# Performance work log

Hardware: AMD Instinct MI355X
Metric: run time of the kernel (lower is better)

## Reference

```python
import jax, jax.numpy as jnp
import numpy as np

WIDTH = 768
HEAD = 64

def setup_inputs() -> dict:
    key = jax.random.key(0)
    ks = jax.random.split(key, 8)
    x = jax.random.normal(ks[0], (8, 2048, WIDTH), dtype=jnp.float32)
    mask = jax.random.randint(ks[1], (2048, 2048), 0, 2, dtype=jnp.int32)
    s = 1.0 / np.sqrt(WIDTH)
    Wq = jax.random.normal(ks[2], (WIDTH, HEAD), dtype=jnp.float32) * s
    Wk = jax.random.normal(ks[3], (WIDTH, HEAD), dtype=jnp.float32) * s
    Wv = jax.random.normal(ks[4], (WIDTH, HEAD), dtype=jnp.float32) * s
    bq = jax.random.normal(ks[5], (HEAD,), dtype=jnp.float32) * 0.01
    bk = jax.random.normal(ks[6], (HEAD,), dtype=jnp.float32) * 0.01
    bv = jax.random.normal(ks[7], (HEAD,), dtype=jnp.float32) * 0.01
    return {"x": x, "Wq": Wq, "bq": bq, "Wk": Wk, "bk": bk, "Wv": Wv, "bv": bv, "mask": mask}

def reference(x, Wq, bq, Wk, bk, Wv, bv, mask) -> jnp.ndarray:
    # x: [B, N, width]; projections -> [B, N, head]
    Q = jnp.einsum('bnw,wh->bnh', x, Wq) + bq
    K = jnp.einsum('bnw,wh->bnh', x, Wk) + bk
    V = jnp.einsum('bnw,wh->bnh', x, Wv) + bv
    scale = 1.0 / jnp.sqrt(jnp.asarray(Q.shape[-1], dtype=Q.dtype))
    scores = jnp.einsum('bqh,bkh->bqk', Q, K) * scale  # [B, N, N]
    scores = jnp.where(mask == 0, -jnp.inf, scores)
    attn = jax.nn.softmax(scores, axis=-1)
    return jnp.einsum('bqk,bkh->bqh', attn, V)
```

## Files before the change

kernel.cpp:

```cpp
#include <hip/hip_runtime.h>

typedef short  s8v   __attribute__((ext_vector_type(8)));
typedef float  f32x4 __attribute__((ext_vector_type(4)));

#define SEQ 2048
#define WID 768

__device__ __forceinline__ unsigned fbits(float f) {
    union { float f; unsigned u; } v; v.f = f; return v.u;
}
__device__ __forceinline__ float bitsf(unsigned u) {
    union { unsigned u; float f; } v; v.u = u; return v.f;
}
__device__ __forceinline__ unsigned short f2b(float f) {
    unsigned u = fbits(f);
    return (unsigned short)((u + 0x7FFFu + ((u >> 16) & 1u)) >> 16);
}
__device__ __forceinline__ unsigned packRNE(float a, float b) {
    unsigned ta = fbits(a) + 0x7FFFu + ((fbits(a) >> 16) & 1u);
    unsigned tb = fbits(b) + 0x7FFFu + ((fbits(b) >> 16) & 1u);
    return __builtin_amdgcn_perm(tb, ta, 0x07060302u);
}
__device__ __forceinline__ unsigned packTRUNC(float a, float b) {
    return __builtin_amdgcn_perm(fbits(b), fbits(a), 0x07060302u);
}
__device__ __forceinline__ f32x4 zero4() { f32x4 z = {0.f, 0.f, 0.f, 0.f}; return z; }

__device__ __forceinline__ void async16(const unsigned short* g, unsigned short* l) {
    __builtin_amdgcn_global_load_lds(
        (const __attribute__((address_space(1))) unsigned int*)g,
        (__attribute__((address_space(3))) unsigned int*)l, 16, 0, 0);
}

__global__ __launch_bounds__(256) void convert_kernel(
    const int* __restrict__ mask,
    const float* __restrict__ Wq, const float* __restrict__ Wk, const float* __restrict__ Wv,
    unsigned short* __restrict__ WF, unsigned* __restrict__ PM)
{
    const int tid = threadIdx.x;
    const int blk = blockIdx.x;
    if (blk < 512) {
        const int gid  = blk * 4 + (tid >> 6);
        const int lane = tid & 63, quad = lane >> 4, c = lane & 15;
        const int qb = gid >> 5, kb = gid & 31;
        unsigned w = 0;
        #pragma unroll
        for (int mt = 0; mt < 2; ++mt) {
            const int q = qb * 32 + mt * 16 + c;
            #pragma unroll
            for (int i = 0; i < 4; ++i) {
                const int4 mm = *(const int4*)&mask[(size_t)q * SEQ + kb * 64 + quad * 16 + 4 * i];
                if (mm.x) w |= 1u << (mt * 16 + i * 4 + 0);
                if (mm.y) w |= 1u << (mt * 16 + i * 4 + 1);
                if (mm.z) w |= 1u << (mt * 16 + i * 4 + 2);
                if (mm.w) w |= 1u << (mt * 16 + i * 4 + 3);
            }
        }
        PM[(size_t)gid * 64 + lane] = w;
    } else {
        const int s2 = (blk - 512) * 256 + tid;
        const int chunk = s2 >> 6, l = s2 & 63;
        const int ntg = chunk / 24, r = chunk - ntg * 24;
        const int kc = r >> 1, h = r & 1;
        const int mat = ntg >> 2;
        const int col = (ntg & 3) * 16 + (l & 15);
        const int k0 = kc * 64 + h * 32 + (l >> 4) * 8;
        const float* Wm = (mat == 0) ? Wq : (mat == 1) ? Wk : Wv;
        float p[8];
        #pragma unroll
        for (int j = 0; j < 8; ++j) p[j] = Wm[(size_t)(k0 + j) * 64 + col];
        uint4 w;
        w.x = packRNE(p[0], p[1]); w.y = packRNE(p[2], p[3]);
        w.z = packRNE(p[4], p[5]); w.w = packRNE(p[6], p[7]);
        *(uint4*)&WF[(size_t)s2 * 8] = w;
    }
}

__global__ __launch_bounds__(512, 4) void qkv_proj_kernel(
    const float* __restrict__ x, const unsigned short* __restrict__ WF,
    const float* __restrict__ bq, const float* __restrict__ bk, const float* __restrict__ bv,
    unsigned short* __restrict__ QF, unsigned short* __restrict__ KF,
    unsigned short* __restrict__ VF)
{
    __shared__ unsigned short AB[2][14336];
    unsigned short (*St)[200] = (unsigned short(*)[200])AB;

    const int tid = threadIdx.x;
    const int wv = tid >> 6, lane = tid & 63, quad = lane >> 4, c = lane & 15;
    const int rg = wv >> 2, cg = wv & 3;
    const int blk = blockIdx.x;
    const int bsw = blk & 7, tsw = blk >> 3;
    const int kbt2 = bsw * 64 + tsw;
    const int kbt  = kbt2 >> 1, hb = kbt2 & 1;
    const int g0r  = kbt2 * 2;

    float bias[3];
    #pragma unroll
    for (int nt = 0; nt < 3; ++nt) {
        int col = cg * 48 + nt * 16 + c;
        const float* B = (col < 64) ? bq : (col < 128) ? bk : bv;
        bias[nt] = B[col & 63];
    }

    const int ach = tid >> 7;
    const int agl = ach >> 1, ah = ach & 1;
    const int al  = (tid >> 1) & 63;
    const int aj0 = (tid & 1) * 4;
    const float* xptr = x + (size_t)((g0r + agl) * 16 + (al & 15)) * WID
                          + ah * 32 + ((al >> 4) & 3) * 8 + aj0;

    auto issueB = [&](int kc, int b) {
        #pragma unroll
        for (int r = 0; r < 3; ++r) {
            const int e = wv * 3 + r;
            const int ntg = e >> 1, h = e & 1;
            async16(WF + (((size_t)ntg * 12 + kc) * 2 + h) * 512 + lane * 8,
                    &AB[b][2048 + (ntg * 2 + h) * 512]);
        }
    };
    auto stageA = [&](int b, float4 f) {
        uint2 w2;
        w2.x = packRNE(f.x, f.y);
        w2.y = packRNE(f.z, f.w);
        *(uint2*)&AB[b][(size_t)tid * 4] = w2;
    };

    f32x4 acc[3];
    #pragma unroll
    for (int nt = 0; nt < 3; ++nt) acc[nt] = zero4();

    {
        float4 f = *(const float4*)&xptr[0];
        stageA(0, f);
        issueB(0, 0);
    }

    for (int kc = 0; kc < 12; ++kc) {
        const int b = kc & 1;
        __syncthreads();
        float4 f;
        if (kc < 11) {
            f = *(const float4*)&xptr[(kc + 1) * 64];
            issueB(kc + 1, b ^ 1);
        }

        s8v afr[2], bfr[3][2];
        #pragma unroll
        for (int h = 0; h < 2; ++h)
            afr[h] = *(const s8v*)&AB[b][(rg * 2 + h) * 512 + lane * 8];
        #pragma unroll
        for (int nt = 0; nt < 3; ++nt)
            #pragma unroll
            for (int h = 0; h < 2; ++h)
                bfr[nt][h] = *(const s8v*)&AB[b][2048 + ((cg * 3 + nt) * 2 + h) * 512 + lane * 8];
        #pragma unroll
        for (int h = 0; h < 2; ++h)
            #pragma unroll
            for (int nt = 0; nt < 3; ++nt)
                acc[nt] = __builtin_amdgcn_mfma_f32_16x16x32_bf16(
                    afr[h], bfr[nt][h], acc[nt], 0, 0, 0);

        if (kc < 11) stageA(b ^ 1, f);
    }

    #pragma unroll
    for (int nt = 0; nt < 3; ++nt)
        #pragma unroll
        for (int i = 0; i < 4; ++i)
            St[rg * 16 + quad * 4 + i][cg * 48 + nt * 16 + c]
                = f2b(acc[nt][i] + bias[nt]);
    __syncthreads();

    if (tid < 256) {
        const int g = tid >> 7, ks = (tid >> 6) & 1, l = tid & 63;
        uint4 v = *(uint4*)&St[g * 16 + (l & 15)][ks * 32 + (l >> 4) * 8];
        *(uint4*)&QF[(((size_t)(g0r + g)) * 2 + ks) * 512 + (size_t)l * 8] = v;
    } else {
        const int t2 = tid - 256;
        const int ksnt = t2 >> 5, idx = t2 & 31;
        const int ks = ksnt >> 2, nt = ksnt & 3;
        const int qd = idx >> 3, ci = idx & 7;
        const int l = qd * 16 + hb * 8 + ci;
        uint4 v = *(uint4*)&St[4 * ci + nt][64 + ks * 32 + qd * 8];
        *(uint4*)&KF[(((size_t)kbt * 8 + ksnt) * 64 + l) * 8] = v;
    }
    if (tid < 256) {
        const int ksnt = tid >> 5, idx = tid & 31;
        const int ks = ksnt >> 2, nt = ksnt & 3;
        const int qd = hb * 2 + (idx >> 4), c2 = idx & 15;
        const int l = qd * 16 + c2;
        const int r0 = (idx >> 4) * 16 + ks * 8;
        const int d = 128 + nt * 16 + c2;
        unsigned short p[8];
        #pragma unroll
        for (int s = 0; s < 8; ++s) p[s] = St[r0 + s][d];
        uint4 w;
        w.x = (unsigned)p[0] | ((unsigned)p[1] << 16);
        w.y = (unsigned)p[2] | ((unsigned)p[3] << 16);
        w.z = (unsigned)p[4] | ((unsigned)p[5] << 16);
        w.w = (unsigned)p[6] | ((unsigned)p[7] << 16);
        *(uint4*)&VF[(((size_t)kbt * 8 + ksnt) * 64 + l) * 8] = w;
    }
}

__global__ __launch_bounds__(1024, 4) void attn_kernel(
    const unsigned short* __restrict__ QF, const unsigned short* __restrict__ KF,
    const unsigned short* __restrict__ VF, const unsigned* __restrict__ PM,
    float* __restrict__ out)
{
    __shared__ float Obuf[64][68];
    __shared__ float Lbuf[64];

    const int tid = threadIdx.x;
    const int wv = tid >> 6, lane = tid & 63, quad = lane >> 4, c = lane & 15;
    const int sl = wv & 3, qg = wv >> 2, mt = qg & 1;
    const int blk = blockIdx.x;
    const int bb = blk & 7, qt = blk >> 3;
    const size_t qrow0 = (size_t)bb * SEQ + qt * 64;

    if (tid < 64) Lbuf[tid] = 0.f;

    union Q8 { s8v v; unsigned w[4]; };
    Q8 qf[2];
    {
        const size_t qgrp = (size_t)bb * 128 + qt * 4 + qg;
        #pragma unroll
        for (int ks = 0; ks < 2; ++ks)
            qf[ks].v = *(const s8v*)&QF[(qgrp * 2 + ks) * 512 + (size_t)lane * 8];
    }

    f32x4 O[4];
    float lro0 = 0.f, lro1 = 0.f;
    #pragma unroll
    for (int nt = 0; nt < 4; ++nt) O[nt] = zero4();

    const unsigned* pmrow = PM + (size_t)((qt * 2 + (qg >> 1)) * 32 + sl * 8) * 64 + lane;

    #pragma unroll 1
    for (int kt = 0; kt < 8; ++kt) {
        const size_t kbg = (size_t)bb * 32 + sl * 8 + kt;
        const unsigned short* kb_ = KF + kbg * 4096 + (size_t)lane * 8;
        const unsigned short* vb_ = VF + kbg * 4096 + (size_t)lane * 8;

        const unsigned pmw = pmrow[(size_t)kt * 64];

        Q8 kf8[8], vf8[8];
        #pragma unroll
        for (int d = 0; d < 8; ++d) kf8[d].v = *(const s8v*)&kb_[(size_t)d * 512];
        #pragma unroll
        for (int d = 0; d < 8; ++d) vf8[d].v = *(const s8v*)&vb_[(size_t)d * 512];

        asm volatile("s_waitcnt vmcnt(8)" ::: "memory");
        #pragma unroll
        for (int d = 0; d < 8; ++d)
            #pragma unroll
            for (int j = 0; j < 4; ++j) asm volatile("" : "+v"(kf8[d].w[j]));
        __builtin_amdgcn_sched_barrier(0);

        f32x4 S[4];
        #pragma unroll
        for (int nt = 0; nt < 4; ++nt) S[nt] = zero4();
        #pragma unroll
        for (int ks = 0; ks < 2; ++ks)
            #pragma unroll
            for (int nt = 0; nt < 4; ++nt)
                S[nt] = __builtin_amdgcn_mfma_f32_16x16x32_bf16(kf8[ks * 4 + nt].v, qf[ks].v, S[nt], 0, 0, 0);

        const unsigned pmh = pmw >> (mt * 16);
        float p[4][4];
        #pragma unroll
        for (int i = 0; i < 4; ++i)
            #pragma unroll
            for (int nt = 0; nt < 4; ++nt) {
                float e = __builtin_amdgcn_exp2f(
                    fmaf(S[nt][i], 0.18033688011112042f, -21.640425613334451f));
                p[nt][i] = ((pmh >> (i * 4 + nt)) & 1u) ? e : 0.f;
            }
        union { unsigned w[8]; s8v v[2]; } P;
        #pragma unroll
        for (int j = 0; j < 8; ++j) {
            unsigned uu = packTRUNC(p[2 * (j & 1)][j >> 1], p[2 * (j & 1) + 1][j >> 1]);
            P.w[j] = uu;
            if (j & 1) lro1 += bitsf(uu << 16) + bitsf(uu & 0xFFFF0000u);
            else       lro0 += bitsf(uu << 16) + bitsf(uu & 0xFFFF0000u);
        }

        asm volatile("s_waitcnt vmcnt(0)" ::: "memory");
        #pragma unroll
        for (int d = 0; d < 8; ++d)
            #pragma unroll
            for (int j = 0; j < 4; ++j) asm volatile("" : "+v"(vf8[d].w[j]));
        __builtin_amdgcn_sched_barrier(0);

        #pragma unroll
        for (int ks = 0; ks < 2; ++ks)
            #pragma unroll
            for (int nt = 0; nt < 4; ++nt)
                O[nt] = __builtin_amdgcn_mfma_f32_16x16x32_bf16(P.v[ks], vf8[ks * 4 + nt].v, O[nt], 0, 0, 0);
    }

    #pragma unroll
    for (int j = 0; j < 5; ++j) {
        int idx = tid + 1024 * j;
        if (idx < 64 * 68) ((float*)Obuf)[idx] = 0.f;
    }
    __syncthreads();

    {
        float l = lro0 + lro1;
        l += __shfl_xor(l, 16);
        l += __shfl_xor(l, 32);
        if (quad == 0) atomicAdd(&Lbuf[qg * 16 + c], l);
    }
    #pragma unroll
    for (int i = 0; i < 4; ++i)
        #pragma unroll
        for (int nt = 0; nt < 4; ++nt)
            atomicAdd(&Obuf[qg * 16 + quad * 4 + i][nt * 16 + c], O[nt][i]);
    __syncthreads();
    {
        const int r = tid >> 4, d4 = (tid & 15) * 4;
        const float invL = 1.0f / Lbuf[r];
        float4 v = *(float4*)&Obuf[r][d4];
        float4 o = make_float4(v.x * invL, v.y * invL, v.z * invL, v.w * invL);
        *(float4*)&out[(qrow0 + r) * 64 + d4] = o;
    }
}

extern "C" void kernel_launch(void* const* d_in, const int* in_sizes, int n_in,
                              void* d_out, int out_size, void* d_ws, size_t ws_size,
                              hipStream_t stream)
{
    const float* x    = (const float*)d_in[0];
    const float* Wq   = (const float*)d_in[1];
    const float* bq   = (const float*)d_in[2];
    const float* Wk   = (const float*)d_in[3];
    const float* bk   = (const float*)d_in[4];
    const float* Wv   = (const float*)d_in[5];
    const float* bv   = (const float*)d_in[6];
    const int*   mask = (const int*)d_in[7];
    float* out = (float*)d_out;

    unsigned short* QF = (unsigned short*)d_ws;
    unsigned short* KF = QF + (size_t)16384 * 64;
    unsigned short* VF = KF + (size_t)16384 * 64;
    unsigned short* WF = VF + (size_t)16384 * 64;
    unsigned*       PM = (unsigned*)(WF + (size_t)192 * WID);

    convert_kernel<<<584, 256, 0, stream>>>(mask, Wq, Wk, Wv, WF, PM);
    qkv_proj_kernel<<<512, 512, 0, stream>>>(x, WF, bq, bk, bv, QF, KF, VF);
    attn_kernel<<<256, 1024, 0, stream>>>(QF, KF, VF, PM, out);
}
```

Baseline: 160.0 us.

## Merge mask packing and QKV projection into one launch, convert weights inline

Folds the mask bit-packing and the QKV projection into a single kernel: the first 256 blocks pack the mask and the remaining 512 blocks run the projection. The separate weight-conversion pass and its bf16 workspace go away. Each projection block now loads fp32 weights with strided scalar global reads and converts them to bf16 in registers, instead of using async global-to-LDS copies of pre-converted weights. This saves one kernel launch and a global round trip. The cost is redundant weight conversion across 512 blocks, uncoalesced weight loads, and more register pressure.

After: 325.7 us. +103.5%, slower.

```diff
diff --git a/kernel.cpp b/kernel.cpp
--- a/kernel.cpp
+++ b/kernel.cpp
@@ -26,22 +26,22 @@
 }
 __device__ __forceinline__ f32x4 zero4() { f32x4 z = {0.f, 0.f, 0.f, 0.f}; return z; }
 
-__device__ __forceinline__ void async16(const unsigned short* g, unsigned short* l) {
-    __builtin_amdgcn_global_load_lds(
-        (const __attribute__((address_space(1))) unsigned int*)g,
-        (__attribute__((address_space(3))) unsigned int*)l, 16, 0, 0);
-}
-
-__global__ __launch_bounds__(256) void convert_kernel(
-    const int* __restrict__ mask,
+__global__ __launch_bounds__(512, 4) void mask_proj_kernel(
+    const float* __restrict__ x, const int* __restrict__ mask,
     const float* __restrict__ Wq, const float* __restrict__ Wk, const float* __restrict__ Wv,
-    unsigned short* __restrict__ WF, unsigned* __restrict__ PM)
+    const float* __restrict__ bq, const float* __restrict__ bk, const float* __restrict__ bv,
+    unsigned short* __restrict__ QF, unsigned short* __restrict__ KF,
+    unsigned short* __restrict__ VF, unsigned* __restrict__ PM)
 {
+    __shared__ unsigned short AB[2][14336];
+    unsigned short (*St)[200] = (unsigned short(*)[200])AB;
+
     const int tid = threadIdx.x;
+    const int wv = tid >> 6, lane = tid & 63, quad = lane >> 4, c = lane & 15;
     const int blk = blockIdx.x;
-    if (blk < 512) {
-        const int gid  = blk * 4 + (tid >> 6);
-        const int lane = tid & 63, quad = lane >> 4, c = lane & 15;
+
+    if (blk < 256) {
+        const int gid = blk * 8 + wv;
         const int qb = gid >> 5, kb = gid & 31;
         unsigned w = 0;
         #pragma unroll
@@ -57,39 +57,12 @@
             }
         }
         PM[(size_t)gid * 64 + lane] = w;
-    } else {
-        const int s2 = (blk - 512) * 256 + tid;
-        const int chunk = s2 >> 6, l = s2 & 63;
-        const int ntg = chunk / 24, r = chunk - ntg * 24;
-        const int kc = r >> 1, h = r & 1;
-        const int mat = ntg >> 2;
-        const int col = (ntg & 3) * 16 + (l & 15);
-        const int k0 = kc * 64 + h * 32 + (l >> 4) * 8;
-        const float* Wm = (mat == 0) ? Wq : (mat == 1) ? Wk : Wv;
-        float p[8];
-        #pragma unroll
-        for (int j = 0; j < 8; ++j) p[j] = Wm[(size_t)(k0 + j) * 64 + col];
-        uint4 w;
-        w.x = packRNE(p[0], p[1]); w.y = packRNE(p[2], p[3]);
-        w.z = packRNE(p[4], p[5]); w.w = packRNE(p[6], p[7]);
-        *(uint4*)&WF[(size_t)s2 * 8] = w;
-    }
-}
-
-__global__ __launch_bounds__(512, 4) void qkv_proj_kernel(
-    const float* __restrict__ x, const unsigned short* __restrict__ WF,
-    const float* __restrict__ bq, const float* __restrict__ bk, const float* __restrict__ bv,
-    unsigned short* __restrict__ QF, unsigned short* __restrict__ KF,
-    unsigned short* __restrict__ VF)
-{
-    __shared__ unsigned short AB[2][14336];
-    unsigned short (*St)[200] = (unsigned short(*)[200])AB;
-
-    const int tid = threadIdx.x;
-    const int wv = tid >> 6, lane = tid & 63, quad = lane >> 4, c = lane & 15;
+        return;
+    }
+
+    const int p = blk - 256;
     const int rg = wv >> 2, cg = wv & 3;
-    const int blk = blockIdx.x;
-    const int bsw = blk & 7, tsw = blk >> 3;
+    const int bsw = p & 7, tsw = p >> 3;
     const int kbt2 = bsw * 64 + tsw;
     const int kbt  = kbt2 >> 1, hb = kbt2 & 1;
     const int g0r  = kbt2 * 2;
@@ -109,13 +82,29 @@
     const float* xptr = x + (size_t)((g0r + agl) * 16 + (al & 15)) * WID
                           + ah * 32 + ((al >> 4) & 3) * 8 + aj0;
 
-    auto issueB = [&](int kc, int b) {
+    float pB[3][8];
+    auto loadB = [&](int kc) {
         #pragma unroll
         for (int r = 0; r < 3; ++r) {
             const int e = wv * 3 + r;
             const int ntg = e >> 1, h = e & 1;
-            async16(WF + (((size_t)ntg * 12 + kc) * 2 + h) * 512 + lane * 8,
-                    &AB[b][2048 + (ntg * 2 + h) * 512]);
+            const int mat = ntg >> 2;
+            const int col = (ntg & 3) * 16 + c;
+            const int k0 = kc * 64 + h * 32 + quad * 8;
+            const float* Wm = (mat == 0) ? Wq : (mat == 1) ? Wk : Wv;
+            #pragma unroll
+            for (int j = 0; j < 8; ++j) pB[r][j] = Wm[(size_t)(k0 + j) * 64 + col];
+        }
+    };
+    auto storeB = [&](int b) {
+        #pragma unroll
+        for (int r = 0; r < 3; ++r) {
+            const int e = wv * 3 + r;
+            const int ntg = e >> 1, h = e & 1;
+            uint4 w;
+            w.x = packRNE(pB[r][0], pB[r][1]); w.y = packRNE(pB[r][2], pB[r][3]);
+            w.z = packRNE(pB[r][4], pB[r][5]); w.w = packRNE(pB[r][6], pB[r][7]);
+            *(uint4*)&AB[b][2048 + (ntg * 2 + h) * 512 + lane * 8] = w;
         }
     };
     auto stageA = [&](int b, float4 f) {
@@ -131,8 +120,9 @@
 
     {
         float4 f = *(const float4*)&xptr[0];
+        loadB(0);
         stageA(0, f);
-        issueB(0, 0);
+        storeB(0);
     }
 
     for (int kc = 0; kc < 12; ++kc) {
@@ -141,7 +131,7 @@
         float4 f;
         if (kc < 11) {
             f = *(const float4*)&xptr[(kc + 1) * 64];
-            issueB(kc + 1, b ^ 1);
+            loadB(kc + 1);
         }
 
         s8v afr[2], bfr[3][2];
@@ -160,7 +150,7 @@
                 acc[nt] = __builtin_amdgcn_mfma_f32_16x16x32_bf16(
                     afr[h], bfr[nt][h], acc[nt], 0, 0, 0);
 
-        if (kc < 11) stageA(b ^ 1, f);
+        if (kc < 11) { stageA(b ^ 1, f); storeB(b ^ 1); }
     }
 
     #pragma unroll
@@ -191,14 +181,14 @@
         const int l = qd * 16 + c2;
         const int r0 = (idx >> 4) * 16 + ks * 8;
         const int d = 128 + nt * 16 + c2;
-        unsigned short p[8];
-        #pragma unroll
-        for (int s = 0; s < 8; ++s) p[s] = St[r0 + s][d];
+        unsigned short pp[8];
+        #pragma unroll
+        for (int s = 0; s < 8; ++s) pp[s] = St[r0 + s][d];
         uint4 w;
-        w.x = (unsigned)p[0] | ((unsigned)p[1] << 16);
-        w.y = (unsigned)p[2] | ((unsigned)p[3] << 16);
-        w.z = (unsigned)p[4] | ((unsigned)p[5] << 16);
-        w.w = (unsigned)p[6] | ((unsigned)p[7] << 16);
+        w.x = (unsigned)pp[0] | ((unsigned)pp[1] << 16);
+        w.y = (unsigned)pp[2] | ((unsigned)pp[3] << 16);
+        w.z = (unsigned)pp[4] | ((unsigned)pp[5] << 16);
+        w.w = (unsigned)pp[6] | ((unsigned)pp[7] << 16);
         *(uint4*)&VF[(((size_t)kbt * 8 + ksnt) * 64 + l) * 8] = w;
     }
 }
@@ -344,10 +334,9 @@
     unsigned short* QF = (unsigned short*)d_ws;
     unsigned short* KF = QF + (size_t)16384 * 64;
     unsigned short* VF = KF + (size_t)16384 * 64;
-    unsigned short* WF = VF + (size_t)16384 * 64;
-    unsigned*       PM = (unsigned*)(WF + (size_t)192 * WID);
-
-    convert_kernel<<<584, 256, 0, stream>>>(mask, Wq, Wk, Wv, WF, PM);
-    qkv_proj_kernel<<<512, 512, 0, stream>>>(x, WF, bq, bk, bv, QF, KF, VF);
+    unsigned*       PM = (unsigned*)(VF + (size_t)16384 * 64);
+
+    mask_proj_kernel<<<768, 512, 0, stream>>>(x, mask, Wq, Wk, Wv, bq, bk, bv,
+                                              QF, KF, VF, PM);
     attn_kernel<<<256, 1024, 0, stream>>>(QF, KF, VF, PM, out);
 }
```
